# Kernel optimization log

Hardware: AMD Instinct MI355X
Metric: run time of the kernel (lower is better)

## Reference

```python
import jax, jax.numpy as jnp
import numpy as np

IN_DIMS = [16, 16, 16]
OUT_DIMS = [16, 16, 16]
RANKS = [1, 16, 16, 1]
BATCH = 1024


def setup_inputs() -> dict:
    key = jax.random.key(0)
    ks = jax.random.split(key, 1 + len(IN_DIMS))
    vector = jax.random.normal(ks[0], (BATCH, *IN_DIMS), dtype=jnp.float32)
    inp = {"vector": vector}
    for i in range(len(IN_DIMS)):
        shape = (RANKS[i], OUT_DIMS[i], IN_DIMS[i], RANKS[i + 1])
        scale = 1.0 / float(np.sqrt(RANKS[i] * IN_DIMS[i]))
        inp[f"core{i}"] = jax.random.normal(ks[1 + i], shape, dtype=jnp.float32) * scale
    return inp


def _tt_matvec(vector, cores):
    """y = M @ x where M is the TT/MPO matrix defined by `cores`.

    vector: (B, d_in_1, ..., d_in_d). Returns (B, d_out_1, ..., d_out_d).
    Mirrors TTMatrix.metric_projection exactly (output dims absorbed into batch).
    """
    bs0 = vector.shape[0]
    res = vector[:, None]  # (B, r0=1, d_in_1, ..., d_in_d)
    bs = bs0
    for core in cores:
        r, o, i, k = core.shape
        rem = res.shape[3:]  # remaining un-contracted input dims
        res_t = res.reshape(bs, r, i, -1)  # (bs, r, i, x)
        # contract rank-in and input dim: (r,o,i,k),(b,r,i,x) -> (b,k,o,x)
        new = jnp.einsum('roik,brix->bkox', core, res_t)
        new = jnp.transpose(new, (0, 2, 1, 3)).reshape(bs * o, k, *rem)
        bs = bs * o
        res = new
    res = jnp.squeeze(res, axis=-1)  # last rank is 1
    out_dims = [c.shape[1] for c in cores]
    return res.reshape(bs0, *out_dims)


def reference(vector, core0, core1, core2):
    return _tt_matvec(vector, (core0, core1, core2))
```

## Files before the change

### kernel.cpp

```cpp
#include <hip/hip_runtime.h>
#include <hip/hip_bf16.h>


typedef short bf16x8 __attribute__((ext_vector_type(8)));
typedef float f32x4 __attribute__((ext_vector_type(4)));

#define WS_A1_OFF 0
#define WS_A0_OFF 131072
#define WS_A2_OFF 147456
#define WS_NEEDED 155648
#define WS2_W12_OFF 0
#define WS2_C2_OFF  2097152
#define WS2_NEEDED  2105344

__device__ __forceinline__ unsigned short f2bf(float f) {
    union { float f; unsigned int u; } x; x.f = f;
    unsigned int u = x.u;
    u += 0x7fffu + ((u >> 16) & 1u);
    return (unsigned short)(u >> 16);
}

__device__ __forceinline__ unsigned int pk_bf16(float lo, float hi) {
    __hip_bfloat162 h = __float22bfloat162_rn(make_float2(lo, hi));
    unsigned int r;
    __builtin_memcpy(&r, &h, 4);
    return r;
}


__global__ void tt_repack2(const float* __restrict__ c0,
                           const float* __restrict__ c1,
                           const float* __restrict__ c2,
                           unsigned short* __restrict__ ws) {
    if (blockIdx.x < 256) {
        int idx = blockIdx.x * 512 + threadIdx.x;
        int mt = idx >> 9, ks = (idx >> 6) & 7, l = idx & 63;
        int o1 = mt >> 4, o2 = mt & 15;
        int k2 = l & 15, lg = l >> 4;
        int i1 = 2 * ks + (lg >> 1);
        int i2b = (lg & 1) * 8;
        float c0row[16];
        #pragma unroll
        for (int k1 = 0; k1 < 16; ++k1) c0row[k1] = c0[o1 * 256 + i1 * 16 + k1];
        unsigned short* dst = ws + ((size_t)(mt * 8 + ks) * 64 + l) * 8;
        #pragma unroll
        for (int j = 0; j < 8; ++j) {
            int i2 = i2b + j;
            float s = 0.f;
            #pragma unroll
            for (int k1 = 0; k1 < 16; ++k1)
                s += c0row[k1] * c1[k1 * 4096 + o2 * 256 + i2 * 16 + k2];
            dst[j] = f2bf(s);
        }
    } else {
        int t = threadIdx.x;
        int ks = t >> 6, l = t & 63;
        unsigned short* dst = ws + WS2_C2_OFF / 2 + ((size_t)ks * 64 + l) * 8;
        #pragma unroll
        for (int j = 0; j < 8; ++j) {
            int k = ks * 32 + ((l >> 4) * 8) + j;
            dst[j] = f2bf(c2[(k & 15) * 256 + (l & 15) * 16 + (k >> 4)]);
        }
    }
}

__global__ __launch_bounds__(512, 2) void tt_main2(
    const float* __restrict__ vg, const unsigned short* __restrict__ ws,
    float* __restrict__ outg)
{
    __shared__ unsigned short vS[16384];
    __shared__ unsigned short T2[2][16384];

    const int b0  = blockIdx.x * 4;
    const int t   = threadIdx.x;
    const int w   = t >> 6;
    const int l   = t & 63;
    const int l15 = l & 15;
    const int lg  = l >> 4;

    bf16x8 fa2[8];
    #pragma unroll
    for (int ks = 0; ks < 8; ++ks)
        fa2[ks] = *(const bf16x8*)(ws + WS2_C2_OFF / 2 + ((size_t)ks * 64 + l) * 8);

    {
        const int bl  = t >> 7;
        const int i3  = (t >> 3) & 15;
        const int i1h = t & 7;
        const float* vb = vg + (size_t)(b0 + bl) * 4096;
        const int rowbyte = (bl * 16 + i3) * 512;
        const int swz = (i3 & 7) << 4;
        #pragma unroll
        for (int q = 0; q < 4; ++q) {
            const int i1  = 2 * i1h + (q >> 1);
            const int i2b = (q & 1) * 8;
            unsigned int pk[4];
            #pragma unroll
            for (int p = 0; p < 4; ++p) {
                float lo = vb[i1 * 256 + (i2b + 2 * p)     * 16 + i3];
                float hi = vb[i1 * 256 + (i2b + 2 * p + 1) * 16 + i3];
                pk[p] = pk_bf16(lo, hi);
            }
            int byte = (rowbyte + (i1 * 16 + i2b) * 2) ^ swz;
            *(uint4*)((char*)vS + byte) = make_uint4(pk[0], pk[1], pk[2], pk[3]);
        }
    }
    __syncthreads();

    bf16x8 fbR[4][8];
    #pragma unroll
    for (int nt = 0; nt < 4; ++nt)
        #pragma unroll
        for (int ks = 0; ks < 8; ++ks) {
            int byte = ((nt * 16 + l15) * 512 + (ks * 32 + lg * 8) * 2) ^ ((l15 & 7) << 4);
            fbR[nt][ks] = *(const bf16x8*)((char*)vS + byte);
        }

    const int o2a = w, o2b = w + 8;

    int curr = 0;
    for (int o1 = 0; o1 < 16; ++o1) {
        bf16x8 fA0[8], fA1[8];
        #pragma unroll
        for (int ks = 0; ks < 8; ++ks) {
            fA0[ks] = *(const bf16x8*)(ws + ((size_t)((o1 * 16 + o2a) * 8 + ks) * 64 + l) * 8);
            fA1[ks] = *(const bf16x8*)(ws + ((size_t)((o1 * 16 + o2b) * 8 + ks) * 64 + l) * 8);
        }

        if (o1 > 0 && w < 4) {
            const unsigned short* T2p = T2[curr ^ 1];
            f32x4 a3a = {0.f, 0.f, 0.f, 0.f};
            f32x4 a3b = {0.f, 0.f, 0.f, 0.f};
            #pragma unroll
            for (int ks3 = 0; ks3 < 8; ks3 += 2) {
                const int i3A = 2 * ks3 + (lg >> 1);
                const int i3B = i3A + 2;
                const int k2b = (lg & 1) * 8;
                int byteA = ((w * 16 + i3A) * 512 + (l15 * 16 + k2b) * 2) ^ ((i3A & 7) << 4);
                int byteB = ((w * 16 + i3B) * 512 + (l15 * 16 + k2b) * 2) ^ ((i3B & 7) << 4);
                bf16x8 fbA = *(const bf16x8*)((char*)T2p + byteA);
                bf16x8 fbB = *(const bf16x8*)((char*)T2p + byteB);
                a3a = __builtin_amdgcn_mfma_f32_16x16x32_bf16(fa2[ks3],     fbA, a3a, 0, 0, 0);
                a3b = __builtin_amdgcn_mfma_f32_16x16x32_bf16(fa2[ks3 + 1], fbB, a3b, 0, 0, 0);
            }
            f32x4 acc3 = a3a + a3b;
            *(f32x4*)(outg + (size_t)(b0 + w) * 4096 + (o1 - 1) * 256 + l15 * 16 + lg * 4) = acc3;
        }

        {
            f32x4 acc[2][4];
            #pragma unroll
            for (int mi = 0; mi < 2; ++mi)
                #pragma unroll
                for (int nt = 0; nt < 4; ++nt) acc[mi][nt] = (f32x4){0.f, 0.f, 0.f, 0.f};

            #pragma unroll
            for (int ks = 0; ks < 8; ++ks) {
                #pragma unroll
                for (int nt = 0; nt < 4; ++nt) {
                    acc[0][nt] = __builtin_amdgcn_mfma_f32_16x16x32_bf16(fA0[ks], fbR[nt][ks], acc[0][nt], 0, 0, 0);
                    acc[1][nt] = __builtin_amdgcn_mfma_f32_16x16x32_bf16(fA1[ks], fbR[nt][ks], acc[1][nt], 0, 0, 0);
                }
            }
            unsigned short* T2c = T2[curr];
            #pragma unroll
            for (int mi = 0; mi < 2; ++mi) {
                const int o2 = mi ? o2b : o2a;
                #pragma unroll
                for (int nt = 0; nt < 4; ++nt) {
                    int byte = ((nt * 16 + l15) * 512 + (o2 * 16 + lg * 4) * 2) ^ ((l15 & 7) << 4);
                    uint2 wv;
                    wv.x = pk_bf16(acc[mi][nt][0], acc[mi][nt][1]);
                    wv.y = pk_bf16(acc[mi][nt][2], acc[mi][nt][3]);
                    *(uint2*)((char*)T2c + byte) = wv;
                }
            }
        }
        __syncthreads();
        curr ^= 1;
    }

    if (w < 4) {
        const unsigned short* T2p = T2[curr ^ 1];
        f32x4 a3a = {0.f, 0.f, 0.f, 0.f};
        f32x4 a3b = {0.f, 0.f, 0.f, 0.f};
        #pragma unroll
        for (int ks3 = 0; ks3 < 8; ks3 += 2) {
            const int i3A = 2 * ks3 + (lg >> 1);
            const int i3B = i3A + 2;
            const int k2b = (lg & 1) * 8;
            int byteA = ((w * 16 + i3A) * 512 + (l15 * 16 + k2b) * 2) ^ ((i3A & 7) << 4);
            int byteB = ((w * 16 + i3B) * 512 + (l15 * 16 + k2b) * 2) ^ ((i3B & 7) << 4);
            bf16x8 fbA = *(const bf16x8*)((char*)T2p + byteA);
            bf16x8 fbB = *(const bf16x8*)((char*)T2p + byteB);
            a3a = __builtin_amdgcn_mfma_f32_16x16x32_bf16(fa2[ks3],     fbA, a3a, 0, 0, 0);
            a3b = __builtin_amdgcn_mfma_f32_16x16x32_bf16(fa2[ks3 + 1], fbB, a3b, 0, 0, 0);
        }
        f32x4 acc3 = a3a + a3b;
        *(f32x4*)(outg + (size_t)(b0 + w) * 4096 + 15 * 256 + l15 * 16 + lg * 4) = acc3;
    }
}


__global__ void tt_repack(const float* __restrict__ c0,
                          const float* __restrict__ c1,
                          const float* __restrict__ c2,
                          unsigned short* __restrict__ ws) {
    int idx = blockIdx.x * 256 + threadIdx.x;
    if (idx < 8192) {
        int o2 = idx >> 9, ks = (idx >> 6) & 7, l = idx & 63;
        int k2 = l & 15;
        unsigned short* dst = ws + ((size_t)(o2 * 8 + ks) * 64 + l) * 8;
        #pragma unroll
        for (int j = 0; j < 8; ++j) {
            int k = ks * 32 + ((l >> 4) * 8) + j;
            dst[j] = f2bf(c1[(k & 15) * 4096 + o2 * 256 + (k >> 4) * 16 + k2]);
        }
    } else if (idx < 9216) {
        int t = idx - 8192;
        int o1 = t >> 6, l = t & 63;
        unsigned short* dst = ws + WS_A0_OFF / 2 + ((size_t)o1 * 64 + l) * 8;
        #pragma unroll
        for (int j = 0; j < 8; ++j) {
            int k = ((l >> 4) * 8) + j;
            float v = (l < 32) ? c0[o1 * 256 + k * 16 + (l & 15)] : 0.f;
            dst[j] = f2bf(v);
        }
    } else if (idx < 9728) {
        int t = idx - 9216;
        int ks = t >> 6, l = t & 63;
        unsigned short* dst = ws + WS_A2_OFF / 2 + ((size_t)ks * 64 + l) * 8;
        #pragma unroll
        for (int j = 0; j < 8; ++j) {
            int k = ks * 32 + ((l >> 4) * 8) + j;
            dst[j] = f2bf(c2[(k & 15) * 256 + (l & 15) * 16 + (k >> 4)]);
        }
    }
}

template <bool PACKED>
__global__ __launch_bounds__(512, 2) void tt_main(
    const float* __restrict__ vg, const float* __restrict__ c0,
    const float* __restrict__ c1, const float* __restrict__ c2,
    const unsigned short* __restrict__ ws, float* __restrict__ outg)
{
    __shared__ unsigned short T1[16384];
    __shared__ unsigned short T2[2][16384];

    const int b = blockIdx.x;
    const int t = threadIdx.x;
    const int w = t >> 6, l = t & 63, l15 = l & 15, lg = l >> 4;
    const int mg = w >> 1, ng = w & 1;

    bf16x8 fb0[2];
    {
        const float* vb = vg + (size_t)b * 4096;
        #pragma unroll
        for (int nt = 0; nt < 2; ++nt) {
            bf16x8 f = {0, 0, 0, 0, 0, 0, 0, 0};
            if (l < 32) {
                int i2 = 2 * w + nt;
                const float* p = vb + (lg * 8) * 256 + i2 * 16 + l15;
                #pragma unroll
                for (int j = 0; j < 8; ++j) f[j] = (short)f2bf(p[j * 256]);
            }
            fb0[nt] = f;
        }
    }
    bf16x8 fa1p[32];
    if constexpr (PACKED) {
        const unsigned short* a1p = ws + (size_t)l * 8;
        #pragma unroll
        for (int rt = 0; rt < 4; ++rt)
            #pragma unroll
            for (int ks = 0; ks < 8; ++ks)
                fa1p[rt * 8 + ks] = *(const bf16x8*)(a1p + ((size_t)((4 * mg + rt) * 8 + ks)) * 512);
    } else {
        for (int rt = 0; rt < 4; ++rt)
            for (int ks = 0; ks < 8; ++ks) {
                int o2 = 4 * mg + rt;
                bf16x8 f;
                for (int j = 0; j < 8; ++j) {
                    int k = ks * 32 + lg * 8 + j;
                    f[j] = (short)f2bf(c1[(k & 15) * 4096 + o2 * 256 + (k >> 4) * 16 + l15]);
                }
                fa1p[rt * 8 + ks] = f;
            }
    }

    for (int nc = 0; nc < 4; ++nc) {
        unsigned short* T2c = T2[nc & 1];
        bf16x8 fa0p[4];
        if constexpr (PACKED) {
            #pragma unroll
            for (int mtl = 0; mtl < 4; ++mtl)
                fa0p[mtl] = *(const bf16x8*)(ws + WS_A0_OFF / 2 +
                                             ((size_t)(nc * 4 + mtl) * 64 + l) * 8);
        } else {
            for (int mtl = 0; mtl < 4; ++mtl) {
                bf16x8 f = {0, 0, 0, 0, 0, 0, 0, 0};
                if (l < 32) {
                    for (int j = 0; j < 8; ++j)
                        f[j] = (short)f2bf(c0[(nc * 4 + mtl) * 256 + (lg * 8 + j) * 16 + l15]);
                }
                fa0p[mtl] = f;
            }
        }
        #pragma unroll
        for (int mtl = 0; mtl < 4; ++mtl) {
            #pragma unroll
            for (int nt = 0; nt < 2; ++nt) {
                f32x4 z = {0.f, 0.f, 0.f, 0.f};
                f32x4 d = __builtin_amdgcn_mfma_f32_16x16x32_bf16(fa0p[mtl], fb0[nt], z, 0, 0, 0);
                const int i2 = 2 * w + nt;
                const int n  = mtl * 16 + l15;
                int byte = (n * 512 + (i2 * 16 + lg * 4) * 2) ^ ((l15 & 7) << 4);
                uint2 wv;
                wv.x = pk_bf16(d[0], d[1]);
                wv.y = pk_bf16(d[2], d[3]);
                *(uint2*)((char*)T1 + byte) = wv;
            }
        }
        __syncthreads();
        {
            f32x4 acc[4][2];
            #pragma unroll
            for (int rt = 0; rt < 4; ++rt)
                #pragma unroll
                for (int ntl = 0; ntl < 2; ++ntl) acc[rt][ntl] = (f32x4){0.f, 0.f, 0.f, 0.f};
            #pragma unroll
            for (int ks = 0; ks < 8; ++ks) {
                #pragma unroll
                for (int ntl = 0; ntl < 2; ++ntl) {
                    const int nt = 2 * ng + ntl;
                    int byte = ((nt * 16 + l15) * 512 + (ks * 32 + lg * 8) * 2) ^ ((l15 & 7) << 4);
                    bf16x8 fb = *(const bf16x8*)((char*)T1 + byte);
                    acc[0][ntl] = __builtin_amdgcn_mfma_f32_16x16x32_bf16(fa1p[0 * 8 + ks], fb, acc[0][ntl], 0, 0, 0);
                    acc[1][ntl] = __builtin_amdgcn_mfma_f32_16x16x32_bf16(fa1p[1 * 8 + ks], fb, acc[1][ntl], 0, 0, 0);
                    acc[2][ntl] = __builtin_amdgcn_mfma_f32_16x16x32_bf16(fa1p[2 * 8 + ks], fb, acc[2][ntl], 0, 0, 0);
                    acc[3][ntl] = __builtin_amdgcn_mfma_f32_16x16x32_bf16(fa1p[3 * 8 + ks], fb, acc[3][ntl], 0, 0, 0);
                }
            }
            #pragma unroll
            for (int rt = 0; rt < 4; ++rt) {
                const int o2 = 4 * mg + rt;
                #pragma unroll
                for (int ntl = 0; ntl < 2; ++ntl) {
                    const int nt = 2 * ng + ntl;
                    int byte = ((nt * 16 + o2) * 512 + (l15 * 16 + lg * 4) * 2) ^ ((o2 & 7) << 4);
                    uint2 wv;
                    wv.x = pk_bf16(acc[rt][ntl][0], acc[rt][ntl][1]);
                    wv.y = pk_bf16(acc[rt][ntl][2], acc[rt][ntl][3]);
                    *(uint2*)((char*)T2c + byte) = wv;
                }
            }
        }
        __syncthreads();
        if (w < 4) {
            bf16x8 fa2[8];
            if constexpr (PACKED) {
                #pragma unroll
                for (int ks = 0; ks < 8; ++ks)
                    fa2[ks] = *(const bf16x8*)(ws + WS_A2_OFF / 2 + ((size_t)ks * 64 + l) * 8);
            } else {
                for (int ks = 0; ks < 8; ++ks) {
                    bf16x8 f;
                    for (int j = 0; j < 8; ++j) {
                        int k = ks * 32 + lg * 8 + j;
                        f[j] = (short)f2bf(c2[(k & 15) * 256 + l15 * 16 + (k >> 4)]);
                    }
                    fa2[ks] = f;
                }
            }
            f32x4 a3a = {0.f, 0.f, 0.f, 0.f};
            f32x4 a3b = {0.f, 0.f, 0.f, 0.f};
            #pragma unroll
            for (int ks = 0; ks < 8; ks += 2) {
                int byte0 = ((w * 16 + l15) * 512 + ((ks + 0) * 32 + lg * 8) * 2) ^ ((l15 & 7) << 4);
                int byte1 = ((w * 16 + l15) * 512 + ((ks + 1) * 32 + lg * 8) * 2) ^ ((l15 & 7) << 4);
                bf16x8 fbA = *(const bf16x8*)((char*)T2c + byte0);
                bf16x8 fbB = *(const bf16x8*)((char*)T2c + byte1);
                a3a = __builtin_amdgcn_mfma_f32_16x16x32_bf16(fa2[ks],     fbA, a3a, 0, 0, 0);
                a3b = __builtin_amdgcn_mfma_f32_16x16x32_bf16(fa2[ks + 1], fbB, a3b, 0, 0, 0);
            }
            f32x4 acc3 = a3a + a3b;
            float* ob = outg + (size_t)b * 4096;
            *(f32x4*)(ob + (nc * 4 + w) * 256 + l15 * 16 + lg * 4) = acc3;
        }
    }
}

extern "C" void kernel_launch(void* const* d_in, const int* in_sizes, int n_in,
                              void* d_out, int out_size, void* d_ws, size_t ws_size,
                              hipStream_t stream) {
    const float* vg  = (const float*)d_in[0];
    const float* c0g = (const float*)d_in[1];
    const float* c1g = (const float*)d_in[2];
    const float* c2g = (const float*)d_in[3];
    float* outg = (float*)d_out;

    const int B = in_sizes[0] / 4096;

    if (ws_size >= (size_t)WS2_NEEDED && d_ws != nullptr && (B % 4) == 0) {
        tt_repack2<<<dim3(257), dim3(512), 0, stream>>>(
            c0g, c1g, c2g, (unsigned short*)d_ws);
        tt_main2<<<dim3(B / 4), dim3(512), 0, stream>>>(
            vg, (const unsigned short*)d_ws, outg);
    } else if (ws_size >= (size_t)WS_NEEDED && d_ws != nullptr) {
        tt_repack<<<dim3(38), dim3(256), 0, stream>>>(c0g, c1g, c2g, (unsigned short*)d_ws);
        tt_main<true><<<dim3(B), dim3(512), 0, stream>>>(
            vg, c0g, c1g, c2g, (const unsigned short*)d_ws, outg);
    } else {
        tt_main<false><<<dim3(B), dim3(512), 0, stream>>>(
            vg, c0g, c1g, c2g, nullptr, outg);
    }
}
```

Baseline: 66.99 us.

## Prefetch next core weights across barrier and stream vS fragments from LDS

Unrolls the o1 loop by two with ping-pong register sets, so each phase loads the next o1's A fragments from global memory while computing the current one. It uses a custom barrier that waits only on LDS counters, leaving those global loads in flight across the barrier. It also drops the 32 persistent vS B-fragment registers and re-reads them from LDS inside the MFMA loop, which frees registers for the extra A buffers at the cost of more LDS traffic.

```diff
diff --git a/kernel.cpp b/kernel.cpp
--- a/kernel.cpp
+++ b/kernel.cpp
@@ -12,6 +12,8 @@
 #define WS2_W12_OFF 0
 #define WS2_C2_OFF  2097152
 #define WS2_NEEDED  2105344
+
+#define BAR_KEEP_LOADS() asm volatile("s_waitcnt lgkmcnt(0)\n\ts_barrier" ::: "memory")
 
 __device__ __forceinline__ unsigned short f2bf(float f) {
     union { float f; unsigned int u; } x; x.f = f;
@@ -64,6 +66,74 @@
     }
 }
 
+__device__ __forceinline__ void tt_phase(
+    int o1, int o1n,
+    const unsigned short* __restrict__ ws, float* __restrict__ outg, int b0,
+    int w, int l, int l15, int lg, int o2a, int o2b,
+    bf16x8 (&fAc0)[8], bf16x8 (&fAc1)[8],
+    bf16x8 (&fAn0)[8], bf16x8 (&fAn1)[8],
+    const bf16x8 (&fa2)[8],
+    const unsigned short* vS, unsigned short* T2w, const unsigned short* T2r)
+{
+    #pragma unroll
+    for (int ks = 0; ks < 8; ++ks) {
+        fAn0[ks] = *(const bf16x8*)(ws + ((size_t)((o1n * 16 + o2a) * 8 + ks) * 64 + l) * 8);
+        fAn1[ks] = *(const bf16x8*)(ws + ((size_t)((o1n * 16 + o2b) * 8 + ks) * 64 + l) * 8);
+    }
+
+    if (o1 > 0 && w < 4) {
+        f32x4 a3a = {0.f, 0.f, 0.f, 0.f};
+        f32x4 a3b = {0.f, 0.f, 0.f, 0.f};
+        #pragma unroll
+        for (int ks3 = 0; ks3 < 8; ks3 += 2) {
+            const int i3A = 2 * ks3 + (lg >> 1);
+            const int i3B = i3A + 2;
+            const int k2b = (lg & 1) * 8;
+            int byteA = ((w * 16 + i3A) * 512 + (l15 * 16 + k2b) * 2) ^ ((i3A & 7) << 4);
+            int byteB = ((w * 16 + i3B) * 512 + (l15 * 16 + k2b) * 2) ^ ((i3B & 7) << 4);
+            bf16x8 fbA = *(const bf16x8*)((const char*)T2r + byteA);
+            bf16x8 fbB = *(const bf16x8*)((const char*)T2r + byteB);
+            a3a = __builtin_amdgcn_mfma_f32_16x16x32_bf16(fa2[ks3],     fbA, a3a, 0, 0, 0);
+            a3b = __builtin_amdgcn_mfma_f32_16x16x32_bf16(fa2[ks3 + 1], fbB, a3b, 0, 0, 0);
+        }
+        f32x4 acc3 = a3a + a3b;
+        *(f32x4*)(outg + (size_t)(b0 + w) * 4096 + (o1 - 1) * 256 + l15 * 16 + lg * 4) = acc3;
+    }
+
+    {
+        f32x4 acc[2][4];
+        #pragma unroll
+        for (int mi = 0; mi < 2; ++mi)
+            #pragma unroll
+            for (int nt = 0; nt < 4; ++nt) acc[mi][nt] = (f32x4){0.f, 0.f, 0.f, 0.f};
+
+        #pragma unroll
+        for (int ks = 0; ks < 8; ++ks) {
+            #pragma unroll
+            for (int nt = 0; nt < 4; ++nt) {
+                int byte = ((nt * 16 + l15) * 512 + (ks * 32 + lg * 8) * 2) ^ ((l15 & 7) << 4);
+                bf16x8 fb = *(const bf16x8*)((const char*)vS + byte);
+                acc[0][nt] = __builtin_amdgcn_mfma_f32_16x16x32_bf16(fAc0[ks], fb, acc[0][nt], 0, 0, 0);
+                acc[1][nt] = __builtin_amdgcn_mfma_f32_16x16x32_bf16(fAc1[ks], fb, acc[1][nt], 0, 0, 0);
+            }
+        }
+        #pragma unroll
+        for (int mi = 0; mi < 2; ++mi) {
+            const int o2 = mi ? o2b : o2a;
+            #pragma unroll
+            for (int nt = 0; nt < 4; ++nt) {
+                int byte = ((nt * 16 + l15) * 512 + (o2 * 16 + lg * 4) * 2) ^ ((l15 & 7) << 4);
+                uint2 wv;
+                wv.x = pk_bf16(acc[mi][nt][0], acc[mi][nt][1]);
+                wv.y = pk_bf16(acc[mi][nt][2], acc[mi][nt][3]);
+                *(uint2*)((char*)T2w + byte) = wv;
+            }
+        }
+    }
+
+    BAR_KEEP_LOADS();
+}
+
 __global__ __launch_bounds__(512, 2) void tt_main2(
     const float* __restrict__ vg, const unsigned short* __restrict__ ws,
     float* __restrict__ outg)
@@ -77,6 +147,7 @@
     const int l   = t & 63;
     const int l15 = l & 15;
     const int lg  = l >> 4;
+    const int o2a = w, o2b = w + 8;
 
     bf16x8 fa2[8];
     #pragma unroll
@@ -105,83 +176,25 @@
             *(uint4*)((char*)vS + byte) = make_uint4(pk[0], pk[1], pk[2], pk[3]);
         }
     }
-    __syncthreads();
-
-    bf16x8 fbR[4][8];
+
+    bf16x8 fAE0[8], fAE1[8], fAO0[8], fAO1[8];
     #pragma unroll
-    for (int nt = 0; nt < 4; ++nt)
-        #pragma unroll
-        for (int ks = 0; ks < 8; ++ks) {
-            int byte = ((nt * 16 + l15) * 512 + (ks * 32 + lg * 8) * 2) ^ ((l15 & 7) << 4);
-            fbR[nt][ks] = *(const bf16x8*)((char*)vS + byte);
-        }
-
-    const int o2a = w, o2b = w + 8;
-
-    int curr = 0;
-    for (int o1 = 0; o1 < 16; ++o1) {
-        bf16x8 fA0[8], fA1[8];
-        #pragma unroll
-        for (int ks = 0; ks < 8; ++ks) {
-            fA0[ks] = *(const bf16x8*)(ws + ((size_t)((o1 * 16 + o2a) * 8 + ks) * 64 + l) * 8);
-            fA1[ks] = *(const bf16x8*)(ws + ((size_t)((o1 * 16 + o2b) * 8 + ks) * 64 + l) * 8);
-        }
-
-        if (o1 > 0 && w < 4) {
-            const unsigned short* T2p = T2[curr ^ 1];
-            f32x4 a3a = {0.f, 0.f, 0.f, 0.f};
-            f32x4 a3b = {0.f, 0.f, 0.f, 0.f};
-            #pragma unroll
-            for (int ks3 = 0; ks3 < 8; ks3 += 2) {
-                const int i3A = 2 * ks3 + (lg >> 1);
-                const int i3B = i3A + 2;
-                const int k2b = (lg & 1) * 8;
-                int byteA = ((w * 16 + i3A) * 512 + (l15 * 16 + k2b) * 2) ^ ((i3A & 7) << 4);
-                int byteB = ((w * 16 + i3B) * 512 + (l15 * 16 + k2b) * 2) ^ ((i3B & 7) << 4);
-                bf16x8 fbA = *(const bf16x8*)((char*)T2p + byteA);
-                bf16x8 fbB = *(const bf16x8*)((char*)T2p + byteB);
-                a3a = __builtin_amdgcn_mfma_f32_16x16x32_bf16(fa2[ks3],     fbA, a3a, 0, 0, 0);
-                a3b = __builtin_amdgcn_mfma_f32_16x16x32_bf16(fa2[ks3 + 1], fbB, a3b, 0, 0, 0);
-            }
-            f32x4 acc3 = a3a + a3b;
-            *(f32x4*)(outg + (size_t)(b0 + w) * 4096 + (o1 - 1) * 256 + l15 * 16 + lg * 4) = acc3;
-        }
-
-        {
-            f32x4 acc[2][4];
-            #pragma unroll
-            for (int mi = 0; mi < 2; ++mi)
-                #pragma unroll
-                for (int nt = 0; nt < 4; ++nt) acc[mi][nt] = (f32x4){0.f, 0.f, 0.f, 0.f};
-
-            #pragma unroll
-            for (int ks = 0; ks < 8; ++ks) {
-                #pragma unroll
-                for (int nt = 0; nt < 4; ++nt) {
-                    acc[0][nt] = __builtin_amdgcn_mfma_f32_16x16x32_bf16(fA0[ks], fbR[nt][ks], acc[0][nt], 0, 0, 0);
-                    acc[1][nt] = __builtin_amdgcn_mfma_f32_16x16x32_bf16(fA1[ks], fbR[nt][ks], acc[1][nt], 0, 0, 0);
-                }
-            }
-            unsigned short* T2c = T2[curr];
-            #pragma unroll
-            for (int mi = 0; mi < 2; ++mi) {
-                const int o2 = mi ? o2b : o2a;
-                #pragma unroll
-                for (int nt = 0; nt < 4; ++nt) {
-                    int byte = ((nt * 16 + l15) * 512 + (o2 * 16 + lg * 4) * 2) ^ ((l15 & 7) << 4);
-                    uint2 wv;
-                    wv.x = pk_bf16(acc[mi][nt][0], acc[mi][nt][1]);
-                    wv.y = pk_bf16(acc[mi][nt][2], acc[mi][nt][3]);
-                    *(uint2*)((char*)T2c + byte) = wv;
-                }
-            }
-        }
-        __syncthreads();
-        curr ^= 1;
+    for (int ks = 0; ks < 8; ++ks) {
+        fAE0[ks] = *(const bf16x8*)(ws + ((size_t)((0 * 16 + o2a) * 8 + ks) * 64 + l) * 8);
+        fAE1[ks] = *(const bf16x8*)(ws + ((size_t)((0 * 16 + o2b) * 8 + ks) * 64 + l) * 8);
+    }
+    BAR_KEEP_LOADS();
+
+    for (int o1o = 0; o1o < 16; o1o += 2) {
+        tt_phase(o1o, o1o + 1, ws, outg, b0, w, l, l15, lg, o2a, o2b,
+                 fAE0, fAE1, fAO0, fAO1, fa2, vS, T2[0], T2[1]);
+        int o1n2 = (o1o + 2 > 15) ? 15 : (o1o + 2);
+        tt_phase(o1o + 1, o1n2, ws, outg, b0, w, l, l15, lg, o2a, o2b,
+                 fAO0, fAO1, fAE0, fAE1, fa2, vS, T2[1], T2[0]);
     }
 
     if (w < 4) {
-        const unsigned short* T2p = T2[curr ^ 1];
+        const unsigned short* T2p = T2[1];
         f32x4 a3a = {0.f, 0.f, 0.f, 0.f};
         f32x4 a3b = {0.f, 0.f, 0.f, 0.f};
         #pragma unroll
@@ -191,8 +204,8 @@
             const int k2b = (lg & 1) * 8;
             int byteA = ((w * 16 + i3A) * 512 + (l15 * 16 + k2b) * 2) ^ ((i3A & 7) << 4);
             int byteB = ((w * 16 + i3B) * 512 + (l15 * 16 + k2b) * 2) ^ ((i3B & 7) << 4);
-            bf16x8 fbA = *(const bf16x8*)((char*)T2p + byteA);
-            bf16x8 fbB = *(const bf16x8*)((char*)T2p + byteB);
+            bf16x8 fbA = *(const bf16x8*)((const char*)T2p + byteA);
+            bf16x8 fbB = *(const bf16x8*)((const char*)T2p + byteB);
             a3a = __builtin_amdgcn_mfma_f32_16x16x32_bf16(fa2[ks3],     fbA, a3a, 0, 0, 0);
             a3b = __builtin_amdgcn_mfma_f32_16x16x32_bf16(fa2[ks3 + 1], fbB, a3b, 0, 0, 0);
         }
```

New measurement: 54.64 us. 18.4% less time.
